# Kernel tuning notes

Hardware: AMD Instinct MI355X
Metric: run time of the kernel (lower is better)

## Reference

```python
import jax, jax.numpy as jnp
import numpy as np

ROUTINGS = 3
NUM_CAPSULE = 32
DIM_CAPSULE = 64


def squash(x, axis=-1):
    # scale = sqrt(||x||^2 + eps) / (0.5 + ||x||^2 + eps)
    sq = jnp.sum(x * x, axis=axis, keepdims=True) + 1e-7
    return (jnp.sqrt(sq) / (0.5 + sq)) * x


def setup_inputs() -> dict:
    key = jax.random.key(0)
    k1, k2 = jax.random.split(key)
    B, IN, ID = 64, 1024, 256
    u_vecs = jax.random.normal(k1, (B, IN, ID), dtype=jnp.float32)
    # nn.Linear weight [NC*DC, ID], xavier_normal init
    fan_out, fan_in = NUM_CAPSULE * DIM_CAPSULE, ID
    std = np.sqrt(2.0 / (fan_in + fan_out)).astype(np.float32)
    W = jax.random.normal(k2, (fan_out, fan_in), dtype=jnp.float32) * std
    return {"u_vecs": u_vecs, "W": W}


def reference(u_vecs, W):
    B, IN, ID = u_vecs.shape
    # Linear projection: [B, IN, NC*DC]
    u_hat = jnp.einsum('bid,od->bio', u_vecs, W)
    # -> [B, NC, IN, DC]
    u_hat = u_hat.reshape(B, IN, NUM_CAPSULE, DIM_CAPSULE).transpose(0, 2, 1, 3)

    b = jnp.zeros((B, NUM_CAPSULE, IN), dtype=u_hat.dtype)
    o = None
    for i in range(ROUTINGS):
        c = jax.nn.softmax(b, axis=1)                      # softmax over output capsules
        o = jnp.einsum('bni,bnid->bnd', c, u_hat)          # [B, NC, DC]
        if i < ROUTINGS - 1:
            # F.normalize(o, 2, -1): x / max(||x||, 1e-12)
            norm = jnp.linalg.norm(o, axis=-1, keepdims=True)
            o = o / jnp.maximum(norm, 1e-12)
            b = jnp.einsum('bnid,bnd->bni', u_hat, o)
    return squash(o)
```

## Files before the change

### kernel.cpp

```cpp
#include <hip/hip_runtime.h>
#include <math.h>


#define B   64
#define IN  1024
#define ID  256
#define NC  32
#define DC  64

__global__ __launch_bounds__(256) void k_sumu(const float* __restrict__ u,
                                              float* __restrict__ sp0) {
    const int c = blockIdx.x, b = blockIdx.y;
    const int d = threadIdx.x;
    const float* up = u + ((size_t)b * IN + (size_t)c * (IN / 8)) * ID + d;
    float acc = 0.f;
#pragma unroll 8
    for (int i = 0; i < IN / 8; ++i) acc += up[(size_t)i * ID];
    sp0[(c * B + b) * ID + d] = acc;
}

__global__ __launch_bounds__(256) void k_ot(const float* __restrict__ W,
                                            const float* __restrict__ src,
                                            float* __restrict__ tout,
                                            const int mode) {
    const int bn = blockIdx.x;
    const int b = bn / NC, n = bn % NC;
    __shared__ float s_lds[ID];
    __shared__ float o_lds[DC];
    __shared__ float on_lds[DC];
    const int tid = threadIdx.x;

    float sv = 0.f;
    if (mode == 0) {
#pragma unroll
        for (int c = 0; c < 8; ++c) sv += src[(c * B + b) * ID + tid];
        sv *= (1.0f / NC);
    } else {
#pragma unroll
        for (int c = 0; c < 8; ++c) sv += src[((size_t)(c * B + b) * NC + n) * ID + tid];
    }
    s_lds[tid] = sv;
    __syncthreads();

    const int wave = tid >> 6, lane = tid & 63;
    const float* Wn = W + (size_t)n * DC * ID;
#pragma unroll 4
    for (int r = 0; r < 16; ++r) {
        const int d = wave * 16 + r;
        const float* wrow = Wn + (size_t)d * ID;
        float p = wrow[lane]        * s_lds[lane]
                + wrow[lane + 64]   * s_lds[lane + 64]
                + wrow[lane + 128]  * s_lds[lane + 128]
                + wrow[lane + 192]  * s_lds[lane + 192];
#pragma unroll
        for (int off = 32; off > 0; off >>= 1) p += __shfl_down(p, off);
        if (lane == 0) o_lds[d] = p;
    }
    __syncthreads();

    if (mode == 2) {
        if (tid < DC) {
            float v = o_lds[tid];
            float sq = v * v;
#pragma unroll
            for (int off = 32; off > 0; off >>= 1) sq += __shfl_down(sq, off);
            sq = __shfl(sq, 0) + 1e-7f;
            const float sc = sqrtf(sq) / (0.5f + sq);
            tout[(size_t)(b * NC + n) * DC + tid] = v * sc;
        }
        return;
    }

    if (tid < DC) {
        float v = o_lds[tid];
        float sq = v * v;
#pragma unroll
        for (int off = 32; off > 0; off >>= 1) sq += __shfl_down(sq, off);
        sq = __shfl(sq, 0);
        const float inv = 1.0f / fmaxf(sqrtf(sq), 1e-12f);
        on_lds[tid] = v * inv;
    }
    __syncthreads();

    float acc = 0.f;
    const float* wc = Wn + tid;
#pragma unroll 8
    for (int d = 0; d < DC; ++d) acc += wc[(size_t)d * ID] * on_lds[d];
    tout[((size_t)b * NC + n) * ID + tid] = acc;
}

#define RTILE 128
__global__ __launch_bounds__(256) void k_route(const float* __restrict__ u,
                                               const float* __restrict__ t,
                                               float* __restrict__ sp) {
    const int it = blockIdx.x, b = blockIdx.y;
    const int iBase = it * RTILE;
    __shared__ float Ts[ID][36];
    __shared__ float Us[16][132];
    __shared__ float cl[RTILE][36];
    const int tid = threadIdx.x;

    {
        const float* tb = t + (size_t)b * NC * ID;
#pragma unroll
        for (int n = 0; n < NC; ++n) Ts[tid][n] = tb[(size_t)n * ID + tid];
    }

    const int q = tid >> 3;
    const int r = tid & 7;
    float acc[4][4] = {{0.f}};
    const float* ub = u + ((size_t)b * IN + iBase) * ID;

    for (int kc = 0; kc < ID / 16; ++kc) {
        __syncthreads();
#pragma unroll
        for (int rep = 0; rep < 2; ++rep) {
            const int f = tid + rep * 256;
            const int i = f >> 2, c4 = f & 3;
            const float4 v = *(const float4*)(ub + (size_t)i * ID + kc * 16 + c4 * 4);
            Us[c4 * 4 + 0][i] = v.x;
            Us[c4 * 4 + 1][i] = v.y;
            Us[c4 * 4 + 2][i] = v.z;
            Us[c4 * 4 + 3][i] = v.w;
        }
        __syncthreads();
#pragma unroll
        for (int k = 0; k < 16; ++k) {
            const float4 a4 = *(const float4*)&Us[k][q * 4];
            const float4 b4 = *(const float4*)&Ts[kc * 16 + k][r * 4];
            const float av[4] = {a4.x, a4.y, a4.z, a4.w};
            const float bv[4] = {b4.x, b4.y, b4.z, b4.w};
#pragma unroll
            for (int ii = 0; ii < 4; ++ii)
#pragma unroll
                for (int jj = 0; jj < 4; ++jj) acc[ii][jj] += av[ii] * bv[jj];
        }
    }

#pragma unroll
    for (int ii = 0; ii < 4; ++ii)
        *(float4*)&cl[q * 4 + ii][r * 4] =
            make_float4(acc[ii][0], acc[ii][1], acc[ii][2], acc[ii][3]);
    __syncthreads();

    {
        const int i = tid >> 1, half = tid & 1;
        float v[16];
#pragma unroll
        for (int j = 0; j < 16; ++j) v[j] = cl[i][half * 16 + j];
        float mx = v[0];
#pragma unroll
        for (int j = 1; j < 16; ++j) mx = fmaxf(mx, v[j]);
        mx = fmaxf(mx, __shfl_xor(mx, 1));
        float sum = 0.f;
#pragma unroll
        for (int j = 0; j < 16; ++j) { v[j] = __expf(v[j] - mx); sum += v[j]; }
        sum += __shfl_xor(sum, 1);
        const float inv = 1.0f / sum;
#pragma unroll
        for (int j = 0; j < 16; ++j) cl[i][half * 16 + j] = v[j] * inv;
    }
    __syncthreads();

    const int d4 = tid & 63;
    const int ng = tid >> 6;
    float a2[8][4] = {{0.f}};
    const float* ur = ub + d4 * 4;
#pragma unroll 4
    for (int i = 0; i < RTILE; ++i) {
        const float4 uv = *(const float4*)(ur + (size_t)i * ID);
        const float4 c0 = *(const float4*)&cl[i][ng * 8];
        const float4 c1 = *(const float4*)&cl[i][ng * 8 + 4];
        const float cv[8] = {c0.x, c0.y, c0.z, c0.w, c1.x, c1.y, c1.z, c1.w};
        const float uvv[4] = {uv.x, uv.y, uv.z, uv.w};
#pragma unroll
        for (int j = 0; j < 8; ++j)
#pragma unroll
            for (int x = 0; x < 4; ++x) a2[j][x] += cv[j] * uvv[x];
    }

    float* spb = sp + (size_t)(it * B + b) * NC * ID;
#pragma unroll
    for (int j = 0; j < 8; ++j) {
        const int n = ng * 8 + j;
        *(float4*)&spb[(size_t)n * ID + d4 * 4] =
            make_float4(a2[j][0], a2[j][1], a2[j][2], a2[j][3]);
    }
}

extern "C" void kernel_launch(void* const* d_in, const int* in_sizes, int n_in,
                              void* d_out, int out_size, void* d_ws, size_t ws_size,
                              hipStream_t stream) {
    const float* u = (const float*)d_in[0];
    const float* W = (const float*)d_in[1];
    float* out = (float*)d_out;

    float* ws  = (float*)d_ws;
    float* t   = ws;
    float* sp  = t + (size_t)B * NC * ID;
    float* sp0 = sp + (size_t)8 * B * NC * ID;

    const dim3 blk(256);

    k_sumu <<<dim3(8, B), blk, 0, stream>>>(u, sp0);
    k_ot   <<<dim3(B * NC), blk, 0, stream>>>(W, sp0, t, 0);
    k_route<<<dim3(IN / RTILE, B), blk, 0, stream>>>(u, t, sp);
    k_ot   <<<dim3(B * NC), blk, 0, stream>>>(W, sp, t, 1);
    k_route<<<dim3(IN / RTILE, B), blk, 0, stream>>>(u, t, sp);
    k_ot   <<<dim3(B * NC), blk, 0, stream>>>(W, sp, out, 2);
}
```

Before: 222.2 us.

## Double-buffer and swizzle shared tiles in routing logits GEMM

Reworks the first phase of k_route, which computes the u·t logits. It now stores t as an XOR-swizzled [NC][ID] shared array with float4 writes. The u tile is prefetched into registers for the next k-chunk and written into a double-buffered, swizzled [RTILE][20] layout, replacing the scalar transposed stores. The inner product now reads float4 along k for both operands. The aim is fewer LDS bank conflicts and less scalar shared-memory traffic, with global-load latency overlapped with compute, at the cost of more registers and a larger shared footprint.

New measurement: 236.7 us. 6.5% more time.

```diff
diff --git a/kernel.cpp b/kernel.cpp
--- a/kernel.cpp
+++ b/kernel.cpp
@@ -95,51 +95,67 @@
                                                float* __restrict__ sp) {
     const int it = blockIdx.x, b = blockIdx.y;
     const int iBase = it * RTILE;
-    __shared__ float Ts[ID][36];
-    __shared__ float Us[16][132];
-    __shared__ float cl[RTILE][36];
+    __shared__ __align__(16) float Tst[NC][ID];
+    __shared__ __align__(16) float Us[2][RTILE][20];
+    __shared__ __align__(16) float cl[RTILE][36];
     const int tid = threadIdx.x;
 
-    {
-        const float* tb = t + (size_t)b * NC * ID;
-#pragma unroll
-        for (int n = 0; n < NC; ++n) Ts[tid][n] = tb[(size_t)n * ID + tid];
+    const float* ub = u + ((size_t)b * IN + iBase) * ID;
+    const float* tb = t + (size_t)b * NC * ID;
+
+#pragma unroll
+    for (int rep = 0; rep < 8; ++rep) {
+        const int idx = tid + rep * 256;
+        const int n = idx >> 6, c4 = idx & 63;
+        const float4 v = *(const float4*)(tb + (size_t)n * ID + c4 * 4);
+        const int c_sw = (c4 * 4) ^ (((n >> 2) & 7) << 2);
+        *(float4*)&Tst[n][c_sw] = v;
     }
 
     const int q = tid >> 3;
     const int r = tid & 7;
+    const int i0 = q * 4, n0 = r * 4;
+    const int si0 = tid >> 2,        sk0 = tid & 3;
+    const int si1 = (tid + 256) >> 2, sk1 = (tid + 256) & 3;
+    const int sc0 = 4 * (sk0 ^ ((si0 >> 2) & 3));
+    const int sc1 = 4 * (sk1 ^ ((si1 >> 2) & 3));
+    const int qs = q & 3;
+
     float acc[4][4] = {{0.f}};
-    const float* ub = u + ((size_t)b * IN + iBase) * ID;
+    float4 pre0 = *(const float4*)(ub + (size_t)si0 * ID + sk0 * 4);
+    float4 pre1 = *(const float4*)(ub + (size_t)si1 * ID + sk1 * 4);
 
     for (int kc = 0; kc < ID / 16; ++kc) {
+        const int buf = kc & 1;
+        *(float4*)&Us[buf][si0][sc0] = pre0;
+        *(float4*)&Us[buf][si1][sc1] = pre1;
         __syncthreads();
-#pragma unroll
-        for (int rep = 0; rep < 2; ++rep) {
-            const int f = tid + rep * 256;
-            const int i = f >> 2, c4 = f & 3;
-            const float4 v = *(const float4*)(ub + (size_t)i * ID + kc * 16 + c4 * 4);
-            Us[c4 * 4 + 0][i] = v.x;
-            Us[c4 * 4 + 1][i] = v.y;
-            Us[c4 * 4 + 2][i] = v.z;
-            Us[c4 * 4 + 3][i] = v.w;
+        if (kc < ID / 16 - 1) {
+            pre0 = *(const float4*)(ub + (size_t)si0 * ID + (kc + 1) * 16 + sk0 * 4);
+            pre1 = *(const float4*)(ub + (size_t)si1 * ID + (kc + 1) * 16 + sk1 * 4);
+        }
+#pragma unroll
+        for (int k4 = 0; k4 < 4; ++k4) {
+            float4 a[4], bv[4];
+            const int ac = 4 * (k4 ^ qs);
+#pragma unroll
+            for (int ii = 0; ii < 4; ++ii) a[ii] = *(const float4*)&Us[buf][i0 + ii][ac];
+            const int bc = (kc * 16 + k4 * 4) ^ (r << 2);
+#pragma unroll
+            for (int jj = 0; jj < 4; ++jj) bv[jj] = *(const float4*)&Tst[n0 + jj][bc];
+#pragma unroll
+            for (int ii = 0; ii < 4; ++ii)
+#pragma unroll
+                for (int jj = 0; jj < 4; ++jj)
+                    acc[ii][jj] += a[ii].x * bv[jj].x + a[ii].y * bv[jj].y
+                                 + a[ii].z * bv[jj].z + a[ii].w * bv[jj].w;
         }
         __syncthreads();
-#pragma unroll
-        for (int k = 0; k < 16; ++k) {
-            const float4 a4 = *(const float4*)&Us[k][q * 4];
-            const float4 b4 = *(const float4*)&Ts[kc * 16 + k][r * 4];
-            const float av[4] = {a4.x, a4.y, a4.z, a4.w};
-            const float bv[4] = {b4.x, b4.y, b4.z, b4.w};
-#pragma unroll
-            for (int ii = 0; ii < 4; ++ii)
-#pragma unroll
-                for (int jj = 0; jj < 4; ++jj) acc[ii][jj] += av[ii] * bv[jj];
-        }
     }
 
 #pragma unroll
     for (int ii = 0; ii < 4; ++ii)
-        *(float4*)&cl[q * 4 + ii][r * 4] =
+        *(float4*)&cl[i0 + ii][n0] =
             make_float4(acc[ii][0], acc[ii][1], acc[ii][2], acc[ii][3]);
     __syncthreads();
 
@@ -200,12 +216,10 @@
     float* sp  = t + (size_t)B * NC * ID;
     float* sp0 = sp + (size_t)8 * B * NC * ID;
 
-    const dim3 blk(256);
-
-    k_sumu <<<dim3(8, B), blk, 0, stream>>>(u, sp0);
-    k_ot   <<<dim3(B * NC), blk, 0, stream>>>(W, sp0, t, 0);
-    k_route<<<dim3(IN / RTILE, B), blk, 0, stream>>>(u, t, sp);
-    k_ot   <<<dim3(B * NC), blk, 0, stream>>>(W, sp, t, 1);
-    k_route<<<dim3(IN / RTILE, B), blk, 0, stream>>>(u, t, sp);
-    k_ot   <<<dim3(B * NC), blk, 0, stream>>>(W, sp, out, 2);
-}
+    k_sumu <<<dim3(8, B), dim3(256), 0, stream>>>(u, sp0);
+    k_ot   <<<dim3(B * NC), dim3(256), 0, stream>>>(W, sp0, t, 0);
+    k_route<<<dim3(IN / RTILE, B), dim3(256), 0, stream>>>(u, t, sp);
+    k_ot   <<<dim3(B * NC), dim3(256), 0, stream>>>(W, sp, t, 1);
+    k_route<<<dim3(IN / RTILE, B), dim3(256), 0, stream>>>(u, t, sp);
+    k_ot   <<<dim3(B * NC), dim3(256), 0, stream>>>(W, sp, out, 2);
+}
```

## Fuse all routing stages into one persistent cooperative kernel with grid syncs

Applied to the files above, without the earlier changes.

Replaces six separate kernel launches with a single cooperative kernel of 512 blocks that runs the sum, projection and routing stages in sequence, separated by grid-wide barriers. Each block handles four projection tasks per iteration and one routing tile. This removes launch gaps and inter-kernel drain, at the cost of grid.sync overhead and keeping all blocks co-resident (launch bounds 256,2). The old multi-kernel path remains as a fallback if the cooperative launch fails.

Measured after the change: 592.2 us. 166% more time.

```diff
diff --git a/kernel.cpp b/kernel.cpp
--- a/kernel.cpp
+++ b/kernel.cpp
@@ -1,5 +1,8 @@
 #include <hip/hip_runtime.h>
+#include <hip/hip_cooperative_groups.h>
 #include <math.h>
+
+namespace cg = cooperative_groups;
 
 
 #define B   64
@@ -7,29 +10,14 @@
 #define ID  256
 #define NC  32
 #define DC  64
-
-__global__ __launch_bounds__(256) void k_sumu(const float* __restrict__ u,
-                                              float* __restrict__ sp0) {
-    const int c = blockIdx.x, b = blockIdx.y;
-    const int d = threadIdx.x;
-    const float* up = u + ((size_t)b * IN + (size_t)c * (IN / 8)) * ID + d;
-    float acc = 0.f;
-#pragma unroll 8
-    for (int i = 0; i < IN / 8; ++i) acc += up[(size_t)i * ID];
-    sp0[(c * B + b) * ID + d] = acc;
-}
-
-__global__ __launch_bounds__(256) void k_ot(const float* __restrict__ W,
-                                            const float* __restrict__ src,
-                                            float* __restrict__ tout,
-                                            const int mode) {
-    const int bn = blockIdx.x;
-    const int b = bn / NC, n = bn % NC;
-    __shared__ float s_lds[ID];
-    __shared__ float o_lds[DC];
-    __shared__ float on_lds[DC];
-    const int tid = threadIdx.x;
-
+#define RTILE 128
+
+__device__ __forceinline__ void ot_body(const float* __restrict__ W,
+                                        const float* __restrict__ src,
+                                        float* __restrict__ dst,
+                                        const int mode, const int b, const int n,
+                                        const int tid,
+                                        float* s_lds, float* o_lds, float* on_lds) {
     float sv = 0.f;
     if (mode == 0) {
 #pragma unroll
@@ -66,7 +54,7 @@
             for (int off = 32; off > 0; off >>= 1) sq += __shfl_down(sq, off);
             sq = __shfl(sq, 0) + 1e-7f;
             const float sc = sqrtf(sq) / (0.5f + sq);
-            tout[(size_t)(b * NC + n) * DC + tid] = v * sc;
+            dst[(size_t)(b * NC + n) * DC + tid] = v * sc;
         }
         return;
     }
@@ -86,30 +74,27 @@
     const float* wc = Wn + tid;
 #pragma unroll 8
     for (int d = 0; d < DC; ++d) acc += wc[(size_t)d * ID] * on_lds[d];
-    tout[((size_t)b * NC + n) * ID + tid] = acc;
-}
-
-#define RTILE 128
-__global__ __launch_bounds__(256) void k_route(const float* __restrict__ u,
-                                               const float* __restrict__ t,
-                                               float* __restrict__ sp) {
-    const int it = blockIdx.x, b = blockIdx.y;
-    const int iBase = it * RTILE;
-    __shared__ float Ts[ID][36];
-    __shared__ float Us[16][132];
-    __shared__ float cl[RTILE][36];
-    const int tid = threadIdx.x;
-
-    {
-        const float* tb = t + (size_t)b * NC * ID;
-#pragma unroll
-        for (int n = 0; n < NC; ++n) Ts[tid][n] = tb[(size_t)n * ID + tid];
-    }
+    dst[((size_t)b * NC + n) * ID + tid] = acc;
+}
+
+__device__ __forceinline__ void route_body(const float* __restrict__ u,
+                                           const float* __restrict__ t,
+                                           float* __restrict__ sp,
+                                           const int it, const int b, const int tid,
+                                           float* smem) {
+    float (*Ts)[36]  = (float(*)[36])smem;
+    float (*Us)[132] = (float(*)[132])(smem + 9216);
+    float (*cl)[36]  = (float(*)[36])(smem + 11328);
+
+    const float* ub = u + ((size_t)b * IN + (size_t)it * RTILE) * ID;
+    const float* tb = t + (size_t)b * NC * ID;
+
+#pragma unroll
+    for (int n = 0; n < NC; ++n) Ts[tid][n] = tb[(size_t)n * ID + tid];
 
     const int q = tid >> 3;
     const int r = tid & 7;
     float acc[4][4] = {{0.f}};
-    const float* ub = u + ((size_t)b * IN + iBase) * ID;
 
     for (int kc = 0; kc < ID / 16; ++kc) {
         __syncthreads();
@@ -181,11 +166,75 @@
 
     float* spb = sp + (size_t)(it * B + b) * NC * ID;
 #pragma unroll
-    for (int j = 0; j < 8; ++j) {
-        const int n = ng * 8 + j;
-        *(float4*)&spb[(size_t)n * ID + d4 * 4] =
+    for (int j = 0; j < 8; ++j)
+        *(float4*)&spb[(size_t)(ng * 8 + j) * ID + d4 * 4] =
             make_float4(a2[j][0], a2[j][1], a2[j][2], a2[j][3]);
-    }
+}
+
+__global__ __launch_bounds__(256, 2) void k_caps(const float* __restrict__ u,
+                                                 const float* __restrict__ W,
+                                                 float* __restrict__ t,
+                                                 float* __restrict__ sp,
+                                                 float* __restrict__ sp0,
+                                                 float* __restrict__ out) {
+    cg::grid_group grid = cg::this_grid();
+    const int bx = blockIdx.x;
+    const int b  = bx & (B - 1);
+    const int it = bx >> 6;
+    const int tid = threadIdx.x;
+    __shared__ __align__(16) float smem[15936];
+
+    {
+        const float* up = u + ((size_t)b * IN + (size_t)it * RTILE) * ID + tid;
+        float a = 0.f;
+#pragma unroll 8
+        for (int i = 0; i < RTILE; ++i) a += up[(size_t)i * ID];
+        sp0[(it * B + b) * ID + tid] = a;
+    }
+    grid.sync();
+
+    for (int iter = 0; iter < 3; ++iter) {
+        const float* src = (iter == 0) ? sp0 : sp;
+        float* dst = (iter == 2) ? out : t;
+#pragma unroll 1
+        for (int j = 0; j < 4; ++j) {
+            const int task = bx * 4 + j;
+            ot_body(W, src, dst, iter, task >> 5, task & (NC - 1), tid,
+                    smem, smem + 256, smem + 320);
+            __syncthreads();
+        }
+        if (iter == 2) break;
+        grid.sync();
+        route_body(u, t, sp, it, b, tid, smem);
+        grid.sync();
+    }
+}
+
+__global__ __launch_bounds__(256) void k_sumu(const float* __restrict__ u,
+                                              float* __restrict__ sp0) {
+    const int c = blockIdx.x, b = blockIdx.y;
+    const int d = threadIdx.x;
+    const float* up = u + ((size_t)b * IN + (size_t)c * RTILE) * ID + d;
+    float acc = 0.f;
+#pragma unroll 8
+    for (int i = 0; i < RTILE; ++i) acc += up[(size_t)i * ID];
+    sp0[(c * B + b) * ID + d] = acc;
+}
+
+__global__ __launch_bounds__(256) void k_ot(const float* __restrict__ W,
+                                            const float* __restrict__ src,
+                                            float* __restrict__ tout,
+                                            const int mode) {
+    __shared__ float smem[384];
+    ot_body(W, src, tout, mode, blockIdx.x / NC, blockIdx.x % NC, threadIdx.x,
+            smem, smem + 256, smem + 320);
+}
+
+__global__ __launch_bounds__(256) void k_route(const float* __restrict__ u,
+                                               const float* __restrict__ t,
+                                               float* __restrict__ sp) {
+    __shared__ __align__(16) float smem[15936];
+    route_body(u, t, sp, blockIdx.x, blockIdx.y, threadIdx.x, smem);
 }
 
 extern "C" void kernel_launch(void* const* d_in, const int* in_sizes, int n_in,
@@ -200,12 +249,16 @@
     float* sp  = t + (size_t)B * NC * ID;
     float* sp0 = sp + (size_t)8 * B * NC * ID;
 
-    const dim3 blk(256);
-
-    k_sumu <<<dim3(8, B), blk, 0, stream>>>(u, sp0);
-    k_ot   <<<dim3(B * NC), blk, 0, stream>>>(W, sp0, t, 0);
-    k_route<<<dim3(IN / RTILE, B), blk, 0, stream>>>(u, t, sp);
-    k_ot   <<<dim3(B * NC), blk, 0, stream>>>(W, sp, t, 1);
-    k_route<<<dim3(IN / RTILE, B), blk, 0, stream>>>(u, t, sp);
-    k_ot   <<<dim3(B * NC), blk, 0, stream>>>(W, sp, out, 2);
-}
+    void* args[] = {(void*)&u, (void*)&W, (void*)&t, (void*)&sp, (void*)&sp0, (void*)&out};
+    const hipError_t err = hipLaunchCooperativeKernel(
+        (const void*)k_caps, dim3(B * (IN / RTILE)), dim3(256), args, 0, stream);
+
+    if (err != hipSuccess) {
+        k_sumu <<<dim3(IN / RTILE, B), dim3(256), 0, stream>>>(u, sp0);
+        k_ot   <<<dim3(B * NC), dim3(256), 0, stream>>>(W, sp0, t, 0);
+        k_route<<<dim3(IN / RTILE, B), dim3(256), 0, stream>>>(u, t, sp);
+        k_ot   <<<dim3(B * NC), dim3(256), 0, stream>>>(W, sp, t, 1);
+        k_route<<<dim3(IN / RTILE, B), dim3(256), 0, stream>>>(u, t, sp);
+        k_ot   <<<dim3(B * NC), dim3(256), 0, stream>>>(W, sp, out, 2);
+    }
+}
```
